# Kernel tuning notes

Measured on AMD Instinct MI355X. Metric: run time of the kernel, lower is better.

The kernel has to match this reference:

```python
import jax, jax.numpy as jnp
import numpy as np

B, N, F_IN, D, TOPK, HID = 64, 512, 256, 128, 20, 512


def setup_inputs() -> dict:
    key = jax.random.key(0)
    ks = jax.random.split(key, 10)
    s = lambda fan: 1.0 / np.sqrt(fan)
    return {
        "data": jax.random.normal(ks[0], (B, F_IN, N), jnp.float32),
        "emb_weight": jax.random.normal(ks[1], (N, D), jnp.float32) * s(D),      # nn.Embedding, kaiming-ish
        "lin_w": jax.random.normal(ks[2], (D, F_IN), jnp.float32) * s(F_IN),     # GraphLayer.lin (no bias)
        "att_i": jax.random.normal(ks[3], (D,), jnp.float32) * 0.1,
        "att_j": jax.random.normal(ks[4], (D,), jnp.float32) * 0.1,
        "att_em_i": jax.random.normal(ks[5], (D,), jnp.float32) * 0.1,
        "att_em_j": jax.random.normal(ks[6], (D,), jnp.float32) * 0.1,
        "gnn_bias": jnp.zeros((D,), jnp.float32),
        "bn_gamma": jnp.ones((D,), jnp.float32),
        "bn_beta": jnp.zeros((D,), jnp.float32),
        "w1": jax.random.normal(ks[7], (HID, N), jnp.float32) * s(N),            # Linear(node_num, hidden, bias=False)
        "w2": jax.random.normal(ks[8], (HID, HID), jnp.float32) * s(HID),        # Linear(hidden, hidden)
        "b2": jnp.zeros((HID,), jnp.float32),
    }


def reference(data, emb_weight, lin_w, att_i, att_j, att_em_i, att_em_j,
              gnn_bias, bn_gamma, bn_beta, w1, w2, b2):
    data = jax.lax.stop_gradient(data)                       # x = data.clone().detach()
    b, f_in, n = data.shape
    d = emb_weight.shape[1]
    x = jnp.transpose(data, (0, 2, 1)).reshape(b * n, f_in)  # [B*N, F]

    # --- dynamic graph from detached embedding: cosine topk ---
    W = jax.lax.stop_gradient(emb_weight)
    nrm = jnp.linalg.norm(W, axis=-1)
    cos = (W @ W.T) / (nrm[:, None] * nrm[None, :])
    topk_idx = jax.lax.top_k(cos, TOPK)[1]                   # [N, topk] (learned_graph)
    src = topk_idx.reshape(-1)                               # gated_j (sources)
    dst = jnp.repeat(jnp.arange(n), TOPK)                    # gated_i (destinations)
    offs = (jnp.arange(b) * n)[:, None]
    bsrc = (src[None, :] + offs).reshape(-1)                 # [B*N*topk]
    bdst = (dst[None, :] + offs).reshape(-1)

    # --- GDN GraphLayer (heads=1, concat=False, aggr=add) ---
    xl = x @ lin_w.T                                         # [B*N, D]
    emb_all = jnp.tile(emb_weight, (b, 1))                   # [B*N, D]
    xi, xj = xl[bdst], xl[bsrc]
    ei, ej = emb_all[bdst], emb_all[bsrc]
    alpha = xi @ att_i + ei @ att_em_i + xj @ att_j + ej @ att_em_j   # [E]
    alpha = jax.nn.leaky_relu(alpha, 0.2)
    amax = jax.ops.segment_max(alpha, bdst, num_segments=b * n)
    ex = jnp.exp(alpha - amax[bdst])
    denom = jax.ops.segment_sum(ex, bdst, num_segments=b * n)
    a = ex / denom[bdst]                                     # segment softmax over dest
    agg = jax.ops.segment_sum(xj * a[:, None], bdst, num_segments=b * n) + gnn_bias

    # --- BatchNorm1d (eval: mean 0, var 1) + ReLU ---
    h = agg * (bn_gamma / jnp.sqrt(1.0 + 1e-5)) + bn_beta
    gcn = jax.nn.relu(h).reshape(b, n, d)

    # --- embedding gate + linear block over node dim ---
    out = gcn * emb_weight[None]                             # [B, N, D]
    out = jnp.transpose(out, (0, 2, 1))                      # [B, D, N]
    out = out @ w1.T                                         # [B, D, HID]
    out = out @ w2.T + b2
    out = jax.nn.sigmoid(out)
    return out, emb_weight, topk_idx
```

## Files before the change

### kernel.cpp

```cpp
#include <hip/hip_runtime.h>
#include <hip/hip_bf16.h>

constexpr int B = 64, N = 512, F_IN = 256, D = 128, TOPK = 20, HID = 512;

typedef __attribute__((ext_vector_type(8))) short short8_t;
typedef __attribute__((ext_vector_type(4))) float f32x4;

__device__ inline short f2bs(float f) {
    union { __hip_bfloat16 h; short s; } u; u.h = __float2bfloat16(f); return u.s;
}
__device__ inline float bs2f(short s) {
    return __uint_as_float(((unsigned)(unsigned short)s) << 16);
}

template<int ITERS>
__device__ inline void stage64_bf16(short* ldst, const short* __restrict__ src,
                                    int stride, int k0, int t) {
    #pragma unroll
    for (int i = 0; i < ITERS; ++i) {
        int lin = t + i * 256, row = lin >> 3, seg = lin & 7;
        *(short8_t*)&ldst[row * 72 + seg * 8] =
            *(const short8_t*)&src[(size_t)row * stride + k0 + seg * 8];
    }
}

template<int MS, int NS>
__device__ inline void mfma_tiles64(const short* lds_a, const short* lds_b,
                                    f32x4 (&acc)[MS][NS], int wm, int wn, int lr, int quad) {
    #pragma unroll
    for (int kc = 0; kc < 64; kc += 32) {
        short8_t af[MS], bf[NS];
        #pragma unroll
        for (int ms = 0; ms < MS; ++ms)
            af[ms] = *(const short8_t*)&lds_a[(wm + ms * 16 + lr) * 72 + kc + quad * 8];
        #pragma unroll
        for (int ns = 0; ns < NS; ++ns)
            bf[ns] = *(const short8_t*)&lds_b[(wn + ns * 16 + lr) * 72 + kc + quad * 8];
        #pragma unroll
        for (int ms = 0; ms < MS; ++ms)
            #pragma unroll
            for (int ns = 0; ns < NS; ++ns)
                acc[ms][ns] = __builtin_amdgcn_mfma_f32_16x16x32_bf16(af[ms], bf[ns], acc[ms][ns], 0, 0, 0);
    }
}

__global__ __launch_bounds__(256) void k_wcvt(const float* __restrict__ lin_w,
                                              const float* __restrict__ w1,
                                              const float* __restrict__ w2,
                                              short* __restrict__ lin_wb,
                                              short* __restrict__ w1b,
                                              short* __restrict__ w2b) {
    int bid = blockIdx.x, t = threadIdx.x;
    const float* src; short* dst; int base;
    if (bid < 16)       { src = lin_w; dst = lin_wb; base = bid * 2048; }
    else if (bid < 144) { src = w1;    dst = w1b;    base = (bid - 16) * 2048; }
    else                { src = w2;    dst = w2b;    base = (bid - 144) * 2048; }
    int idx = base + t * 8;
    float4 x = *(const float4*)(src + idx), y = *(const float4*)(src + idx + 4);
    short8_t v = { f2bs(x.x), f2bs(x.y), f2bs(x.z), f2bs(x.w),
                   f2bs(y.x), f2bs(y.y), f2bs(y.z), f2bs(y.w) };
    *(short8_t*)(dst + idx) = v;
}

__global__ void k_norm(const float* __restrict__ W, const float* __restrict__ aei,
                       const float* __restrict__ aej, float* __restrict__ inv_norm,
                       float* __restrict__ ei, float* __restrict__ ej,
                       float* __restrict__ out_emb) {
    int n = blockIdx.x, t = threadIdx.x;
    float w = W[n * D + t];
    out_emb[n * D + t] = w;
    float s0 = w * w, s1 = w * aei[t], s2 = w * aej[t];
    #pragma unroll
    for (int o = 32; o > 0; o >>= 1) {
        s0 += __shfl_down(s0, o); s1 += __shfl_down(s1, o); s2 += __shfl_down(s2, o);
    }
    __shared__ float r[6];
    if ((t & 63) == 0) { int q = t >> 6; r[q * 3] = s0; r[q * 3 + 1] = s1; r[q * 3 + 2] = s2; }
    __syncthreads();
    if (t == 0) {
        inv_norm[n] = 1.0f / sqrtf(r[0] + r[3]);
        ei[n] = r[1] + r[4];
        ej[n] = r[2] + r[5];
    }
}

__global__ __launch_bounds__(256) void k_cos(const float* __restrict__ W,
                                             const float* __restrict__ inv_norm,
                                             float* __restrict__ cosm) {
    __shared__ float la[32][33];
    __shared__ float lb[32][33];
    int j0 = blockIdx.x * 32, i0 = blockIdx.y * 32, t = threadIdx.x;
    int ix = (t & 15) * 2, jx = (t >> 4) * 2;
    float acc[2][2] = {};
    for (int k0 = 0; k0 < D; k0 += 32) {
        #pragma unroll
        for (int i = 0; i < 4; ++i) {
            int lin = t + i * 256, rl = lin & 31, kk = lin >> 5;
            la[kk][rl] = W[(size_t)(i0 + rl) * D + k0 + kk];
            lb[kk][rl] = W[(size_t)(j0 + rl) * D + k0 + kk];
        }
        __syncthreads();
        #pragma unroll
        for (int kk = 0; kk < 32; ++kk) {
            float a0 = la[kk][ix], a1 = la[kk][ix + 1];
            float b0 = lb[kk][jx], b1 = lb[kk][jx + 1];
            acc[0][0] += a0 * b0; acc[0][1] += a0 * b1;
            acc[1][0] += a1 * b0; acc[1][1] += a1 * b1;
        }
        __syncthreads();
    }
    #pragma unroll
    for (int ii = 0; ii < 2; ++ii) {
        float inv_i = inv_norm[i0 + ix + ii];
        float2 v;
        v.x = acc[ii][0] * inv_i * inv_norm[j0 + jx + 0];
        v.y = acc[ii][1] * inv_i * inv_norm[j0 + jx + 1];
        *(float2*)&cosm[(size_t)(i0 + ix + ii) * N + j0 + jx] = v;
    }
}

__global__ __launch_bounds__(256) void k_sel(const float* __restrict__ cosm,
                                             int* __restrict__ topk,
                                             float* __restrict__ out_idx) {
    int t = threadIdx.x, wid = t >> 6, lane = t & 63;
    int i = blockIdx.x * 4 + wid;
    float4 p0 = *(const float4*)&cosm[(size_t)i * N + lane * 8];
    float4 p1 = *(const float4*)&cosm[(size_t)i * N + lane * 8 + 4];
    float v[8] = {p0.x, p0.y, p0.z, p0.w, p1.x, p1.y, p1.z, p1.w};
    for (int k = 0; k < TOPK; ++k) {
        float bv = v[0]; int bc = 0;
        #pragma unroll
        for (int c = 1; c < 8; ++c) if (v[c] > bv) { bv = v[c]; bc = c; }
        int bj = lane * 8 + bc;
        #pragma unroll
        for (int o = 1; o < 64; o <<= 1) {
            float ov = __shfl_xor(bv, o);
            int  oj = __shfl_xor(bj, o);
            if (ov > bv || (ov == bv && oj < bj)) { bv = ov; bj = oj; }
        }
        if (lane == 0) {
            topk[i * TOPK + k] = bj;
            out_idx[i * TOPK + k] = (float)bj;
        }
        int oc = bj & 7; bool owner = (bj >> 3) == lane;
        #pragma unroll
        for (int c = 0; c < 8; ++c) if (owner && c == oc) v[c] = -INFINITY;
    }
}

__global__ __launch_bounds__(256) void k_xl(const float* __restrict__ data,
                                            const short* __restrict__ lin_wb,
                                            const float* __restrict__ att_i,
                                            const float* __restrict__ att_j,
                                            const float* __restrict__ ei,
                                            const float* __restrict__ ej,
                                            short* __restrict__ xlb,
                                            float* __restrict__ s_i,
                                            float* __restrict__ s_j) {
    __shared__ float lt[64][33];
    __shared__ __align__(16) short lds_a[32 * 72];
    __shared__ __align__(16) short lds_b[128 * 72];
    __shared__ float sred[2][32][2];
    int n0 = blockIdx.x * 32, b = blockIdx.y, t = threadIdx.x;
    int wid = t >> 6, lane = t & 63;
    int wm = (wid & 1) * 16, wn = (wid >> 1) * 64;
    int lr = lane & 15, quad = lane >> 4;
    f32x4 acc[1][4] = {};
    for (int k0 = 0; k0 < F_IN; k0 += 64) {
        {
            int f = t >> 2, ng = (t & 3) * 8;
            const float* p = &data[((size_t)b * F_IN + k0 + f) * N + n0 + ng];
            float4 v0 = *(const float4*)p, v1 = *(const float4*)(p + 4);
            float* q = &lt[f][ng];
            q[0] = v0.x; q[1] = v0.y; q[2] = v0.z; q[3] = v0.w;
            q[4] = v1.x; q[5] = v1.y; q[6] = v1.z; q[7] = v1.w;
        }
        stage64_bf16<4>(lds_b, lin_wb, F_IN, k0, t);
        __syncthreads();
        {
            int row = t >> 3, seg = t & 7;
            short8_t a;
            #pragma unroll
            for (int j = 0; j < 8; ++j) a[j] = f2bs(lt[seg * 8 + j][row]);
            *(short8_t*)&lds_a[row * 72 + seg * 8] = a;
        }
        __syncthreads();
        mfma_tiles64<1, 4>(lds_a, lds_b, acc, wm, wn, lr, quad);
        __syncthreads();
    }
    #pragma unroll
    for (int ns = 0; ns < 4; ++ns) {
        int mb = wm + quad * 4, col = wn + ns * 16 + lr;
        #pragma unroll
        for (int r = 0; r < 4; ++r)
            xlb[((size_t)b * N + n0 + mb + r) * D + col] = f2bs(acc[0][ns][r]);
    }
    float si4[4], sj4[4];
    #pragma unroll
    for (int r = 0; r < 4; ++r) {
        float si = 0.f, sj = 0.f;
        #pragma unroll
        for (int ns = 0; ns < 4; ++ns) {
            int col = wn + ns * 16 + lr;
            float x = acc[0][ns][r];
            si += x * att_i[col];
            sj += x * att_j[col];
        }
        si4[r] = si; sj4[r] = sj;
    }
    #pragma unroll
    for (int o = 1; o < 16; o <<= 1) {
        #pragma unroll
        for (int i = 0; i < 4; ++i) {
            si4[i] += __shfl_xor(si4[i], o);
            sj4[i] += __shfl_xor(sj4[i], o);
        }
    }
    if (lr == 0) {
        #pragma unroll
        for (int r = 0; r < 4; ++r) {
            int row = wm + quad * 4 + r;
            sred[wid >> 1][row][0] = si4[r];
            sred[wid >> 1][row][1] = sj4[r];
        }
    }
    __syncthreads();
    if (t < 32) {
        int n = n0 + t;
        s_i[b * N + n] = sred[0][t][0] + sred[1][t][0] + ei[n];
        s_j[b * N + n] = sred[0][t][1] + sred[1][t][1] + ej[n];
    }
}

__global__ __launch_bounds__(256) void k_attn2(const short* __restrict__ xlb,
                                               const float* __restrict__ emb,
                                               const int* __restrict__ topk,
                                               const float* __restrict__ s_i,
                                               const float* __restrict__ s_j,
                                               const float* __restrict__ gnn_bias,
                                               const float* __restrict__ bn_gamma,
                                               const float* __restrict__ bn_beta,
                                               short* __restrict__ Gt) {
    __shared__ float alph[16][20];
    __shared__ int   js[16][20];
    __shared__ float lt[16][129];
    int n0 = blockIdx.x * 16, b = blockIdx.y, t = threadIdx.x;
    for (int e = t; e < 16 * TOPK; e += 256) {
        int nl = e / TOPK, k = e - nl * TOPK;
        int j = topk[(n0 + nl) * TOPK + k];
        js[nl][k] = j;
        float al = s_i[b * N + n0 + nl] + s_j[b * N + j];
        alph[nl][k] = al >= 0.f ? al : 0.2f * al;
    }
    __syncthreads();
    if (t < 16) {
        float m = -INFINITY;
        for (int k = 0; k < TOPK; ++k) m = fmaxf(m, alph[t][k]);
        float s = 0.f;
        for (int k = 0; k < TOPK; ++k) { float e_ = expf(alph[t][k] - m); alph[t][k] = e_; s += e_; }
        float inv = 1.0f / s;
        for (int k = 0; k < TOPK; ++k) alph[t][k] *= inv;
    }
    __syncthreads();
    {
        int nl = t >> 4, dl = (t & 15) * 8;
        float a[8] = {};
        for (int k = 0; k < TOPK; ++k) {
            float w = alph[nl][k];
            short8_t xv = *(const short8_t*)&xlb[((size_t)b * N + js[nl][k]) * D + dl];
            #pragma unroll
            for (int c = 0; c < 8; ++c) a[c] += w * bs2f(xv[c]);
        }
        const float bnk = 0.9999950000374997f;
        #pragma unroll
        for (int c = 0; c < 8; ++c) {
            int d = dl + c;
            float h = (a[c] + gnn_bias[d]) * (bn_gamma[d] * bnk) + bn_beta[d];
            h = fmaxf(h, 0.f);
            lt[nl][d] = h * emb[(n0 + nl) * D + d];
        }
    }
    __syncthreads();
    {
        int d = t >> 1, half = t & 1;
        short8_t v;
        #pragma unroll
        for (int j = 0; j < 8; ++j) v[j] = f2bs(lt[half * 8 + j][d]);
        *(short8_t*)&Gt[((size_t)b * D + d) * N + n0 + half * 8] = v;
    }
}

__global__ __launch_bounds__(256) void k_gemm1(const short* __restrict__ Gt,
                                               const short* __restrict__ w1b,
                                               short* __restrict__ out1) {
    __shared__ __align__(16) short lds_a[64 * 72];
    __shared__ __align__(16) short lds_b[64 * 72];
    int h0 = blockIdx.x * 64, d0 = blockIdx.y * 64, b = blockIdx.z, t = threadIdx.x;
    int wid = t >> 6, lane = t & 63;
    int wm = (wid >> 1) * 32, wn = (wid & 1) * 32;
    int lr = lane & 15, quad = lane >> 4;
    f32x4 acc[2][2] = {};
    const short* Asrc = Gt + ((size_t)b * D + d0) * N;
    const short* Bsrc = w1b + (size_t)h0 * N;
    for (int k0 = 0; k0 < N; k0 += 64) {
        stage64_bf16<2>(lds_a, Asrc, N, k0, t);
        stage64_bf16<2>(lds_b, Bsrc, N, k0, t);
        __syncthreads();
        mfma_tiles64<2, 2>(lds_a, lds_b, acc, wm, wn, lr, quad);
        __syncthreads();
    }
    #pragma unroll
    for (int ms = 0; ms < 2; ++ms)
        #pragma unroll
        for (int ns = 0; ns < 2; ++ns) {
            int mb = d0 + wm + ms * 16 + quad * 4, col = h0 + wn + ns * 16 + lr;
            #pragma unroll
            for (int r = 0; r < 4; ++r)
                out1[((size_t)b * D + mb + r) * HID + col] = f2bs(acc[ms][ns][r]);
        }
}

__global__ __launch_bounds__(256) void k_gemm2(const short* __restrict__ out1,
                                               const short* __restrict__ w2b,
                                               const float* __restrict__ b2,
                                               float* __restrict__ out) {
    __shared__ __align__(16) short lds_a[64 * 72];
    __shared__ __align__(16) short lds_b[64 * 72];
    int h0 = blockIdx.x * 64, d0 = blockIdx.y * 64, b = blockIdx.z, t = threadIdx.x;
    int wid = t >> 6, lane = t & 63;
    int wm = (wid >> 1) * 32, wn = (wid & 1) * 32;
    int lr = lane & 15, quad = lane >> 4;
    f32x4 acc[2][2] = {};
    const short* Asrc = out1 + ((size_t)b * D + d0) * HID;
    const short* Bsrc = w2b + (size_t)h0 * HID;
    for (int k0 = 0; k0 < HID; k0 += 64) {
        stage64_bf16<2>(lds_a, Asrc, HID, k0, t);
        stage64_bf16<2>(lds_b, Bsrc, HID, k0, t);
        __syncthreads();
        mfma_tiles64<2, 2>(lds_a, lds_b, acc, wm, wn, lr, quad);
        __syncthreads();
    }
    #pragma unroll
    for (int ms = 0; ms < 2; ++ms)
        #pragma unroll
        for (int ns = 0; ns < 2; ++ns) {
            int mb = d0 + wm + ms * 16 + quad * 4, col = h0 + wn + ns * 16 + lr;
            float bias = b2[col];
            #pragma unroll
            for (int r = 0; r < 4; ++r)
                out[((size_t)b * D + mb + r) * HID + col] =
                    1.0f / (1.0f + expf(-(acc[ms][ns][r] + bias)));
        }
}

extern "C" void kernel_launch(void* const* d_in, const int* in_sizes, int n_in,
                              void* d_out, int out_size, void* d_ws, size_t ws_size,
                              hipStream_t stream) {
    const float* data     = (const float*)d_in[0];
    const float* emb      = (const float*)d_in[1];
    const float* lin_w    = (const float*)d_in[2];
    const float* att_i    = (const float*)d_in[3];
    const float* att_j    = (const float*)d_in[4];
    const float* att_em_i = (const float*)d_in[5];
    const float* att_em_j = (const float*)d_in[6];
    const float* gnn_bias = (const float*)d_in[7];
    const float* bn_gamma = (const float*)d_in[8];
    const float* bn_beta  = (const float*)d_in[9];
    const float* w1       = (const float*)d_in[10];
    const float* w2       = (const float*)d_in[11];
    const float* b2       = (const float*)d_in[12];
    float* out            = (float*)d_out;

    float* ws       = (float*)d_ws;
    float* inv_norm = ws;
    float* ei       = ws + 512;
    float* ej       = ws + 1024;
    int*   topk     = (int*)(ws + 1536);
    float* s_i      = ws + 1536 + N * TOPK;
    float* s_j      = s_i + B * N;
    short* lin_wb   = (short*)(ws + 77312);
    short* w1b      = lin_wb + D * F_IN;
    short* w2b      = w1b + HID * N;
    short* S        = w2b + HID * HID;
    short* Gt       = S;
    short* out1     = S + (size_t)B * D * N;
    short* xlb      = S + 2 * (size_t)B * D * N;
    float* cosm     = (float*)S;

    float* out_emb = out + (size_t)B * D * HID;
    float* out_idx = out_emb + (size_t)N * D;

    hipLaunchKernelGGL(k_wcvt,  dim3(272),            dim3(256), 0, stream, lin_w, w1, w2, lin_wb, w1b, w2b);
    hipLaunchKernelGGL(k_norm,  dim3(N),              dim3(D),   0, stream, emb, att_em_i, att_em_j, inv_norm, ei, ej, out_emb);
    hipLaunchKernelGGL(k_cos,   dim3(N / 32, N / 32), dim3(256), 0, stream, emb, inv_norm, cosm);
    hipLaunchKernelGGL(k_sel,   dim3(N / 4),          dim3(256), 0, stream, cosm, topk, out_idx);
    hipLaunchKernelGGL(k_xl,    dim3(N / 32, B),      dim3(256), 0, stream, data, lin_wb, att_i, att_j, ei, ej, xlb, s_i, s_j);
    hipLaunchKernelGGL(k_attn2, dim3(N / 16, B),      dim3(256), 0, stream, xlb, emb, topk, s_i, s_j, gnn_bias, bn_gamma, bn_beta, Gt);
    hipLaunchKernelGGL(k_gemm1, dim3(HID / 64, D / 64, B), dim3(256), 0, stream, Gt, w1b, out1);
    hipLaunchKernelGGL(k_gemm2, dim3(HID / 64, D / 64, B), dim3(256), 0, stream, out1, w2b, b2, out);
}
```

Baseline: 182.7 us.

## Stage GEMM tiles with direct global-to-LDS loads into XOR-swizzled layout

Replaces register-staged global->LDS copies in the xl, gemm1 and gemm2 kernels with global_load_lds 16-byte direct loads. The LDS tiles drop the padded 72-stride layout for a dense 64-stride layout with an XOR swizzle on 16-byte chunks, which keeps bank conflicts down on the MFMA fragment reads. This removes the VGPR round trip and padding in LDS. It relies on correct wait semantics for async LDS loads before the barrier.

```diff
diff --git a/kernel.cpp b/kernel.cpp
--- a/kernel.cpp
+++ b/kernel.cpp
@@ -13,35 +13,25 @@
     return __uint_as_float(((unsigned)(unsigned short)s) << 16);
 }
 
-template<int ITERS>
-__device__ inline void stage64_bf16(short* ldst, const short* __restrict__ src,
-                                    int stride, int k0, int t) {
-    #pragma unroll
-    for (int i = 0; i < ITERS; ++i) {
-        int lin = t + i * 256, row = lin >> 3, seg = lin & 7;
-        *(short8_t*)&ldst[row * 72 + seg * 8] =
-            *(const short8_t*)&src[(size_t)row * stride + k0 + seg * 8];
-    }
-}
-
-template<int MS, int NS>
-__device__ inline void mfma_tiles64(const short* lds_a, const short* lds_b,
-                                    f32x4 (&acc)[MS][NS], int wm, int wn, int lr, int quad) {
-    #pragma unroll
-    for (int kc = 0; kc < 64; kc += 32) {
-        short8_t af[MS], bf[NS];
-        #pragma unroll
-        for (int ms = 0; ms < MS; ++ms)
-            af[ms] = *(const short8_t*)&lds_a[(wm + ms * 16 + lr) * 72 + kc + quad * 8];
-        #pragma unroll
-        for (int ns = 0; ns < NS; ++ns)
-            bf[ns] = *(const short8_t*)&lds_b[(wn + ns * 16 + lr) * 72 + kc + quad * 8];
-        #pragma unroll
-        for (int ms = 0; ms < MS; ++ms)
-            #pragma unroll
-            for (int ns = 0; ns < NS; ++ns)
-                acc[ms][ns] = __builtin_amdgcn_mfma_f32_16x16x32_bf16(af[ms], bf[ns], acc[ms][ns], 0, 0, 0);
-    }
+__device__ inline void gll16(const void* gptr, void* lptr) {
+    __builtin_amdgcn_global_load_lds(
+        (const __attribute__((address_space(1))) unsigned*)gptr,
+        (__attribute__((address_space(3))) unsigned*)lptr, 16, 0, 0);
+}
+
+template<int CH>
+__device__ inline void stage_sw(short* lds, const short* __restrict__ src,
+                                int stride, int k0, int wid, int lane) {
+    int r8 = lane >> 3, cc = (lane & 7) ^ r8;
+    #pragma unroll
+    for (int i = 0; i < CH / 4; ++i) {
+        int ch = wid * (CH / 4) + i;
+        gll16(&src[(size_t)(ch * 8 + r8) * stride + k0 + cc * 8], &lds[ch * 512]);
+    }
+}
+
+__device__ inline short8_t ld_sw(const short* lds, int row, int c16) {
+    return *(const short8_t*)&lds[row * 64 + ((c16 ^ (row & 7)) << 3)];
 }
 
 __global__ __launch_bounds__(256) void k_wcvt(const float* __restrict__ lin_w,
@@ -159,14 +149,15 @@
                                             float* __restrict__ s_j) {
     __shared__ float lt[64][33];
     __shared__ __align__(16) short lds_a[32 * 72];
-    __shared__ __align__(16) short lds_b[128 * 72];
+    __shared__ __align__(16) short lds_b[128 * 64];
     __shared__ float sred[2][32][2];
     int n0 = blockIdx.x * 32, b = blockIdx.y, t = threadIdx.x;
     int wid = t >> 6, lane = t & 63;
     int wm = (wid & 1) * 16, wn = (wid >> 1) * 64;
     int lr = lane & 15, quad = lane >> 4;
-    f32x4 acc[1][4] = {};
+    f32x4 acc[4] = {};
     for (int k0 = 0; k0 < F_IN; k0 += 64) {
+        stage_sw<16>(lds_b, lin_wb, F_IN, k0, wid, lane);
         {
             int f = t >> 2, ng = (t & 3) * 8;
             const float* p = &data[((size_t)b * F_IN + k0 + f) * N + n0 + ng];
@@ -175,7 +166,6 @@
             q[0] = v0.x; q[1] = v0.y; q[2] = v0.z; q[3] = v0.w;
             q[4] = v1.x; q[5] = v1.y; q[6] = v1.z; q[7] = v1.w;
         }
-        stage64_bf16<4>(lds_b, lin_wb, F_IN, k0, t);
         __syncthreads();
         {
             int row = t >> 3, seg = t & 7;
@@ -185,7 +175,16 @@
             *(short8_t*)&lds_a[row * 72 + seg * 8] = a;
         }
         __syncthreads();
-        mfma_tiles64<1, 4>(lds_a, lds_b, acc, wm, wn, lr, quad);
+        #pragma unroll
+        for (int kc = 0; kc < 64; kc += 32) {
+            int cb = quad + (kc >> 3);
+            short8_t a = *(const short8_t*)&lds_a[(wm + lr) * 72 + kc + quad * 8];
+            #pragma unroll
+            for (int ns = 0; ns < 4; ++ns) {
+                short8_t bfr = ld_sw(lds_b, wn + ns * 16 + lr, cb);
+                acc[ns] = __builtin_amdgcn_mfma_f32_16x16x32_bf16(a, bfr, acc[ns], 0, 0, 0);
+            }
+        }
         __syncthreads();
     }
     #pragma unroll
@@ -193,7 +192,7 @@
         int mb = wm + quad * 4, col = wn + ns * 16 + lr;
         #pragma unroll
         for (int r = 0; r < 4; ++r)
-            xlb[((size_t)b * N + n0 + mb + r) * D + col] = f2bs(acc[0][ns][r]);
+            xlb[((size_t)b * N + n0 + mb + r) * D + col] = f2bs(acc[ns][r]);
     }
     float si4[4], sj4[4];
     #pragma unroll
@@ -202,7 +201,7 @@
         #pragma unroll
         for (int ns = 0; ns < 4; ++ns) {
             int col = wn + ns * 16 + lr;
-            float x = acc[0][ns][r];
+            float x = acc[ns][r];
             si += x * att_i[col];
             sj += x * att_j[col];
         }
@@ -293,8 +292,8 @@
 __global__ __launch_bounds__(256) void k_gemm1(const short* __restrict__ Gt,
                                                const short* __restrict__ w1b,
                                                short* __restrict__ out1) {
-    __shared__ __align__(16) short lds_a[64 * 72];
-    __shared__ __align__(16) short lds_b[64 * 72];
+    __shared__ __align__(16) short lds_a[64 * 64];
+    __shared__ __align__(16) short lds_b[64 * 64];
     int h0 = blockIdx.x * 64, d0 = blockIdx.y * 64, b = blockIdx.z, t = threadIdx.x;
     int wid = t >> 6, lane = t & 63;
     int wm = (wid >> 1) * 32, wn = (wid & 1) * 32;
@@ -303,10 +302,23 @@
     const short* Asrc = Gt + ((size_t)b * D + d0) * N;
     const short* Bsrc = w1b + (size_t)h0 * N;
     for (int k0 = 0; k0 < N; k0 += 64) {
-        stage64_bf16<2>(lds_a, Asrc, N, k0, t);
-        stage64_bf16<2>(lds_b, Bsrc, N, k0, t);
-        __syncthreads();
-        mfma_tiles64<2, 2>(lds_a, lds_b, acc, wm, wn, lr, quad);
+        stage_sw<8>(lds_a, Asrc, N, k0, wid, lane);
+        stage_sw<8>(lds_b, Bsrc, N, k0, wid, lane);
+        __syncthreads();
+        #pragma unroll
+        for (int kc = 0; kc < 64; kc += 32) {
+            int cb = quad + (kc >> 3);
+            short8_t af[2], bf[2];
+            #pragma unroll
+            for (int ms = 0; ms < 2; ++ms) af[ms] = ld_sw(lds_a, wm + ms * 16 + lr, cb);
+            #pragma unroll
+            for (int ns = 0; ns < 2; ++ns) bf[ns] = ld_sw(lds_b, wn + ns * 16 + lr, cb);
+            #pragma unroll
+            for (int ms = 0; ms < 2; ++ms)
+                #pragma unroll
+                for (int ns = 0; ns < 2; ++ns)
+                    acc[ms][ns] = __builtin_amdgcn_mfma_f32_16x16x32_bf16(af[ms], bf[ns], acc[ms][ns], 0, 0, 0);
+        }
         __syncthreads();
     }
     #pragma unroll
@@ -324,8 +336,8 @@
                                                const short* __restrict__ w2b,
                                                const float* __restrict__ b2,
                                                float* __restrict__ out) {
-    __shared__ __align__(16) short lds_a[64 * 72];
-    __shared__ __align__(16) short lds_b[64 * 72];
+    __shared__ __align__(16) short lds_a[64 * 64];
+    __shared__ __align__(16) short lds_b[64 * 64];
     int h0 = blockIdx.x * 64, d0 = blockIdx.y * 64, b = blockIdx.z, t = threadIdx.x;
     int wid = t >> 6, lane = t & 63;
     int wm = (wid >> 1) * 32, wn = (wid & 1) * 32;
@@ -334,10 +346,23 @@
     const short* Asrc = out1 + ((size_t)b * D + d0) * HID;
     const short* Bsrc = w2b + (size_t)h0 * HID;
     for (int k0 = 0; k0 < HID; k0 += 64) {
-        stage64_bf16<2>(lds_a, Asrc, HID, k0, t);
-        stage64_bf16<2>(lds_b, Bsrc, HID, k0, t);
-        __syncthreads();
-        mfma_tiles64<2, 2>(lds_a, lds_b, acc, wm, wn, lr, quad);
+        stage_sw<8>(lds_a, Asrc, HID, k0, wid, lane);
+        stage_sw<8>(lds_b, Bsrc, HID, k0, wid, lane);
+        __syncthreads();
+        #pragma unroll
+        for (int kc = 0; kc < 64; kc += 32) {
+            int cb = quad + (kc >> 3);
+            short8_t af[2], bf[2];
+            #pragma unroll
+            for (int ms = 0; ms < 2; ++ms) af[ms] = ld_sw(lds_a, wm + ms * 16 + lr, cb);
+            #pragma unroll
+            for (int ns = 0; ns < 2; ++ns) bf[ns] = ld_sw(lds_b, wn + ns * 16 + lr, cb);
+            #pragma unroll
+            for (int ms = 0; ms < 2; ++ms)
+                #pragma unroll
+                for (int ns = 0; ns < 2; ++ns)
+                    acc[ms][ns] = __builtin_amdgcn_mfma_f32_16x16x32_bf16(af[ms], bf[ns], acc[ms][ns], 0, 0, 0);
+        }
         __syncthreads();
     }
     #pragma unroll
```

New measurement: 185.0 us. No clear change (+1.3%).
